# Kernel tuning notes

Hardware: AMD Instinct MI355X
Metric: run time of the kernel (lower is better)

## Reference

```python
import jax, jax.numpy as jnp
import numpy as np

DD = 2.5
GAMMA = 0.005


def setup_inputs() -> dict:
    key = jax.random.key(0)
    k1, k2 = jax.random.split(key)
    B, C, H, W = 8, 32, 512, 512
    K = 16
    features_batch = jax.random.normal(k1, (B, C, H, W), dtype=jnp.float32)
    labels_batch = jax.random.randint(k2, (B, H, W), 0, K, dtype=jnp.int64)
    return {"features_batch": features_batch, "labels_batch": labels_batch, "num_instances": K}


def _per_image_loss(f, lab, K):
    # f: [N, C], lab: [N] int in [0, K)
    counts = jax.ops.segment_sum(jnp.ones(lab.shape, f.dtype), lab, num_segments=K)  # [K]
    sums = jax.ops.segment_sum(f, lab, num_segments=K)                               # [K, C]
    means = sums / counts[:, None]                                                   # [K, C]
    # variance term: mean over pixels of ||x - mean_cluster||^2, summed over clusters
    d2 = jnp.sum((f - means[lab]) ** 2, axis=1)                                      # [N]
    var_loss = jnp.sum(jax.ops.segment_sum(d2, lab, num_segments=K) / counts)
    # pairwise hinge distance term over i<j
    diff2 = jnp.sum((means[:, None, :] - means[None, :, :]) ** 2, axis=-1)           # [K, K]
    eye = jnp.eye(K, dtype=bool)
    dist = jnp.sqrt(jnp.where(eye, 1.0, diff2))  # safe sqrt on diagonal
    hinge = jnp.maximum(2.0 * DD - dist, 0.0) ** 2
    pair_mask = jnp.triu(jnp.ones((K, K), dtype=bool), k=1)
    dist_loss = jnp.sum(jnp.where(pair_mask, hinge, 0.0)) / (K - 1)
    # regularizer: sum of L2 norms of cluster means
    reg_loss = jnp.sum(jnp.sqrt(jnp.sum(means ** 2, axis=-1)))
    return (var_loss + dist_loss + GAMMA * reg_loss) / K


def reference(features_batch, labels_batch, num_instances):
    B, C, H, W = features_batch.shape
    K = int(num_instances)
    feats = jnp.transpose(features_batch, (0, 2, 3, 1)).reshape(B, H * W, C)
    labs = labels_batch.reshape(B, H * W)
    losses = jax.vmap(lambda f, l: _per_image_loss(f, l, K))(feats, labs)  # [B]
    return jnp.sum(losses) / (B + 1)
```

## Files before the change

### kernel.cpp

```cpp
#include <hip/hip_runtime.h>

#define NPIX (512*512)
#define CCH 32
#define KCL 16
#define TPIX 4096
#define BLKT 512
#define STEPS (TPIX/256)
#define WS_STRIDE 544


template<bool WITH_CNT>
__device__ __forceinline__ void run_tile(const float* __restrict__ f0,
    const float* __restrict__ f1, const float* __restrict__ f2,
    const float* __restrict__ f3, const unsigned char* slab, int lane,
    float acc[4][KCL], float* sqa, float* cnt)
{
  #pragma unroll 2
  for (int s = 0; s < STEPS; ++s) {
    const int p = s * 256 + lane * 4;
    const unsigned int labw = *reinterpret_cast<const unsigned int*>(slab + p);
    const float4 a0 = *reinterpret_cast<const float4*>(f0 + p);
    const float4 a1 = *reinterpret_cast<const float4*>(f1 + p);
    const float4 a2 = *reinterpret_cast<const float4*>(f2 + p);
    const float4 a3 = *reinterpret_cast<const float4*>(f3 + p);
    const float va0[4] = {a0.x, a0.y, a0.z, a0.w};
    const float va1[4] = {a1.x, a1.y, a1.z, a1.w};
    const float va2[4] = {a2.x, a2.y, a2.z, a2.w};
    const float va3[4] = {a3.x, a3.y, a3.z, a3.w};
    #pragma unroll
    for (int px = 0; px < 4; ++px) {
      const int lab = (int)((labw >> (8 * px)) & 0xFF);
      const float v0 = va0[px], v1 = va1[px], v2 = va2[px], v3 = va3[px];
      float sq = v0 * v0;
      sq = fmaf(v1, v1, sq);
      sq = fmaf(v2, v2, sq);
      sq = fmaf(v3, v3, sq);
      #pragma unroll
      for (int k = 0; k < KCL; ++k) {
        const float m = (lab == k) ? 1.0f : 0.0f;
        acc[0][k] = fmaf(m, v0, acc[0][k]);
        acc[1][k] = fmaf(m, v1, acc[1][k]);
        acc[2][k] = fmaf(m, v2, acc[2][k]);
        acc[3][k] = fmaf(m, v3, acc[3][k]);
        sqa[k]    = fmaf(m, sq, sqa[k]);
        if (WITH_CNT) cnt[k] += m;
      }
    }
  }
}

#define RS_LEVEL(ARR, HALF, MASK) { \
    const bool hi = (lane & (MASK)) != 0; \
    _Pragma("unroll") \
    for (int j = 0; j < (HALF); ++j) { \
      float send = hi ? ARR[j] : ARR[j + (HALF)]; \
      float recv = __shfl_xor(send, (MASK), 64); \
      ARR[j] = (hi ? ARR[j + (HALF)] : ARR[j]) + recv; \
    } }

__global__ void __launch_bounds__(BLKT)
cl_accum_kernel(const float* __restrict__ feats, const int* __restrict__ labs,
                float* __restrict__ ws)
{
  const int b    = blockIdx.x >> 6;
  const int tile = blockIdx.x & 63;
  const int tid  = threadIdx.x;
  const int wave = tid >> 6;
  const int lane = tid & 63;
  const int px0  = tile * TPIX;

  __shared__ unsigned char slab[TPIX];
  const int* lb = labs + b * NPIX + px0;
  #pragma unroll
  for (int i = 0; i < TPIX / BLKT; ++i)
    slab[tid + i * BLKT] = (unsigned char)lb[tid + i * BLKT];
  __syncthreads();

  const float* fbase = feats + ((long long)b * CCH) * NPIX + px0;
  const float* f0 = fbase + (long long)(wave     ) * NPIX;
  const float* f1 = fbase + (long long)(wave +  8) * NPIX;
  const float* f2 = fbase + (long long)(wave + 16) * NPIX;
  const float* f3 = fbase + (long long)(wave + 24) * NPIX;

  float acc[4][KCL];
  float sqa[KCL], cnt[KCL];
  #pragma unroll
  for (int ch = 0; ch < 4; ++ch)
    #pragma unroll
    for (int k = 0; k < KCL; ++k) acc[ch][k] = 0.f;
  #pragma unroll
  for (int k = 0; k < KCL; ++k) { sqa[k] = 0.f; cnt[k] = 0.f; }

  if (wave == 0) run_tile<true >(f0, f1, f2, f3, slab, lane, acc, sqa, cnt);
  else           run_tile<false>(f0, f1, f2, f3, slab, lane, acc, sqa, cnt);

  float a[64];
  #pragma unroll
  for (int ch = 0; ch < 4; ++ch)
    #pragma unroll
    for (int k = 0; k < KCL; ++k) a[ch * 16 + k] = acc[ch][k];

  RS_LEVEL(a, 32,  1)
  RS_LEVEL(a, 16,  2)
  RS_LEVEL(a,  8,  4)
  RS_LEVEL(a,  4,  8)
  RS_LEVEL(a,  2, 16)
  RS_LEVEL(a,  1, 32)

  {
    const int v6  = (int)(__brev((unsigned)lane) >> 26);
    const int chl = v6 >> 4, k = v6 & 15;
    const int c   = wave + chl * 8;
    atomicAdd(&ws[b * WS_STRIDE + 32 + k * 32 + c], a[0]);
  }

  float bb[32];
  #pragma unroll
  for (int k = 0; k < KCL; ++k) { bb[k] = sqa[k]; bb[16 + k] = cnt[k]; }
  RS_LEVEL(bb, 16,  1)
  RS_LEVEL(bb,  8,  2)
  RS_LEVEL(bb,  4,  4)
  RS_LEVEL(bb,  2,  8)
  RS_LEVEL(bb,  1, 16)
  bb[0] += __shfl_xor(bb[0], 32, 64);
  if (lane < 32) {
    const int v5 = (int)(__brev((unsigned)(lane)) >> 27);
    if (v5 < 16) atomicAdd(&ws[b * WS_STRIDE + 16 + v5], bb[0]);
    else if (wave == 0) atomicAdd(&ws[b * WS_STRIDE + (v5 - 16)], bb[0]);
  }
}

__global__ void __launch_bounds__(512)
cl_finalize_kernel(const float* __restrict__ ws, float* __restrict__ out)
{
  __shared__ float smean[8][KCL][33];
  __shared__ float slossb[8];
  const int tid  = threadIdx.x;
  const int w    = tid >> 6;
  const int lane = tid & 63;
  const float* base = ws + w * WS_STRIDE;

  float m2part = 0.f;
  #pragma unroll
  for (int j = 0; j < 8; ++j) {
    const int idx = lane * 8 + j;
    const int k = idx >> 5, c = idx & 31;
    const float m = base[32 + k * 32 + c] / base[k];
    smean[w][k][c] = m;
    m2part = fmaf(m, m, m2part);
  }
  float varp = -m2part;
  if (lane < 16) varp += base[16 + lane] / base[lane];
  #pragma unroll
  for (int mk = 1; mk < 64; mk <<= 1) varp += __shfl_xor(varp, mk, 64);

  __syncthreads();

  const int kk = lane >> 2, q = lane & 3;
  float n2 = 0.f;
  #pragma unroll
  for (int j = 0; j < 8; ++j) {
    const float m = smean[w][kk][q * 8 + j];
    n2 = fmaf(m, m, n2);
  }
  n2 += __shfl_xor(n2, 1, 64);
  n2 += __shfl_xor(n2, 2, 64);
  float regp = (q == 0) ? sqrtf(n2) : 0.f;
  #pragma unroll
  for (int mk = 1; mk < 64; mk <<= 1) regp += __shfl_xor(regp, mk, 64);

  float hing = 0.f;
  for (int p = lane; p < 120; p += 64) {
    int i = 0, rem = p;
    while (rem >= 15 - i) { rem -= 15 - i; ++i; }
    const int jj = i + 1 + rem;
    float d2 = 0.f;
    #pragma unroll
    for (int c = 0; c < 32; ++c) {
      const float d = smean[w][i][c] - smean[w][jj][c];
      d2 = fmaf(d, d, d2);
    }
    const float h = fmaxf(5.0f - sqrtf(d2), 0.f);
    hing = fmaf(h, h, hing);
  }
  #pragma unroll
  for (int mk = 1; mk < 64; mk <<= 1) hing += __shfl_xor(hing, mk, 64);

  if (lane == 0)
    slossb[w] = (varp + hing * (1.0f / 15.0f) + 0.005f * regp) * (1.0f / 16.0f);
  __syncthreads();
  if (tid == 0) {
    float t = 0.f;
    #pragma unroll
    for (int i = 0; i < 8; ++i) t += slossb[i];
    out[0] = t * (1.0f / 9.0f);
  }
}

extern "C" void kernel_launch(void* const* d_in, const int* in_sizes, int n_in,
                              void* d_out, int out_size, void* d_ws, size_t ws_size,
                              hipStream_t stream)
{
  const float* feats = (const float*)d_in[0];
  const int*   labs  = (const int*)d_in[1];
  float* out = (float*)d_out;
  float* ws  = (float*)d_ws;

  hipMemsetAsync(d_ws, 0, 8 * WS_STRIDE * sizeof(float), stream);
  hipLaunchKernelGGL(cl_accum_kernel, dim3(512), dim3(BLKT), 0, stream,
                     feats, labs, ws);
  hipLaunchKernelGGL(cl_finalize_kernel, dim3(1), dim3(512), 0, stream,
                     ws, out);
}
```

Measured before the change: 77.13 us.

## Distribute label counting across all waves and raise occupancy via launch bounds

Label counts used to be accumulated only by wave 0 inside the main loop, which made that wave do extra work and kept 16 more live registers. Now every thread counts 8 labels from the shared slab after the main loop, and all waves contribute count atomics. __launch_bounds__(BLKT, 4) is added to ask the compiler to limit registers so more blocks can be resident. The risk is register spilling, given the 80+ accumulators per thread, plus more atomics per block.

Result: slower. 130.7 us (+69.4%).

```diff
diff --git a/kernel.cpp b/kernel.cpp
--- a/kernel.cpp
+++ b/kernel.cpp
@@ -9,11 +9,10 @@
 #define WS_STRIDE 544
 
 
-template<bool WITH_CNT>
 __device__ __forceinline__ void run_tile(const float* __restrict__ f0,
     const float* __restrict__ f1, const float* __restrict__ f2,
     const float* __restrict__ f3, const unsigned char* slab, int lane,
-    float acc[4][KCL], float* sqa, float* cnt)
+    float acc[4][KCL], float* sqa)
 {
   #pragma unroll 2
   for (int s = 0; s < STEPS; ++s) {
@@ -43,7 +42,6 @@
         acc[2][k] = fmaf(m, v2, acc[2][k]);
         acc[3][k] = fmaf(m, v3, acc[3][k]);
         sqa[k]    = fmaf(m, sq, sqa[k]);
-        if (WITH_CNT) cnt[k] += m;
       }
     }
   }
@@ -58,7 +56,7 @@
       ARR[j] = (hi ? ARR[j + (HALF)] : ARR[j]) + recv; \
     } }
 
-__global__ void __launch_bounds__(BLKT)
+__global__ void __launch_bounds__(BLKT, 4)
 cl_accum_kernel(const float* __restrict__ feats, const int* __restrict__ labs,
                 float* __restrict__ ws)
 {
@@ -83,16 +81,33 @@
   const float* f3 = fbase + (long long)(wave + 24) * NPIX;
 
   float acc[4][KCL];
-  float sqa[KCL], cnt[KCL];
+  float sqa[KCL];
   #pragma unroll
   for (int ch = 0; ch < 4; ++ch)
     #pragma unroll
     for (int k = 0; k < KCL; ++k) acc[ch][k] = 0.f;
   #pragma unroll
-  for (int k = 0; k < KCL; ++k) { sqa[k] = 0.f; cnt[k] = 0.f; }
-
-  if (wave == 0) run_tile<true >(f0, f1, f2, f3, slab, lane, acc, sqa, cnt);
-  else           run_tile<false>(f0, f1, f2, f3, slab, lane, acc, sqa, cnt);
+  for (int k = 0; k < KCL; ++k) sqa[k] = 0.f;
+
+  run_tile(f0, f1, f2, f3, slab, lane, acc, sqa);
+
+  float cnt[KCL];
+  #pragma unroll
+  for (int k = 0; k < KCL; ++k) cnt[k] = 0.f;
+  {
+    const unsigned int w0 = *reinterpret_cast<const unsigned int*>(slab + tid * 8);
+    const unsigned int w1 = *reinterpret_cast<const unsigned int*>(slab + tid * 8 + 4);
+    #pragma unroll
+    for (int j = 0; j < 4; ++j) {
+      const int l0 = (int)((w0 >> (8 * j)) & 0xFF);
+      const int l1 = (int)((w1 >> (8 * j)) & 0xFF);
+      #pragma unroll
+      for (int k = 0; k < KCL; ++k) {
+        cnt[k] += (l0 == k) ? 1.0f : 0.0f;
+        cnt[k] += (l1 == k) ? 1.0f : 0.0f;
+      }
+    }
+  }
 
   float a[64];
   #pragma unroll
@@ -126,7 +141,7 @@
   if (lane < 32) {
     const int v5 = (int)(__brev((unsigned)(lane)) >> 27);
     if (v5 < 16) atomicAdd(&ws[b * WS_STRIDE + 16 + v5], bb[0]);
-    else if (wave == 0) atomicAdd(&ws[b * WS_STRIDE + (v5 - 16)], bb[0]);
+    else         atomicAdd(&ws[b * WS_STRIDE + (v5 - 16)], bb[0]);
   }
 }
 
```

## Precompute label histogram and fold per-cluster variance into weighted scalar sum

Applied to the files above, without the earlier changes.

Adds a separate histogram kernel that counts labels per image before the main pass. The accumulation kernel then weights each pixel's squared norm by 1/count for its cluster and sums into one scalar, so the 16 per-cluster square-sum and count accumulators and their reductions go away. This lowers register pressure and VALU work in the inner loop, and launch bounds now request 4 waves per SIMD. The cost is an extra kernel launch plus a second read of the labels, and per-pixel weights staged in LDS.

After: 74.42 us. -3.5%, faster.

```diff
diff --git a/kernel.cpp b/kernel.cpp
--- a/kernel.cpp
+++ b/kernel.cpp
@@ -8,17 +8,86 @@
 #define STEPS (TPIX/256)
 #define WS_STRIDE 544
 
-
-template<bool WITH_CNT>
-__device__ __forceinline__ void run_tile(const float* __restrict__ f0,
-    const float* __restrict__ f1, const float* __restrict__ f2,
-    const float* __restrict__ f3, const unsigned char* slab, int lane,
-    float acc[4][KCL], float* sqa, float* cnt)
-{
+#define RS_LEVEL(ARR, HALF, MASK) { \
+    const bool hi = (lane & (MASK)) != 0; \
+    _Pragma("unroll") \
+    for (int j = 0; j < (HALF); ++j) { \
+      float send = hi ? ARR[j] : ARR[j + (HALF)]; \
+      float recv = __shfl_xor(send, (MASK), 64); \
+      ARR[j] = (hi ? ARR[j + (HALF)] : ARR[j]) + recv; \
+    } }
+
+__global__ void __launch_bounds__(512)
+cl_hist_kernel(const int* __restrict__ labs, float* __restrict__ ws)
+{
+  const int b    = blockIdx.x >> 4;
+  const int seg  = blockIdx.x & 15;
+  const int tid  = threadIdx.x;
+  const int lane = tid & 63;
+  const int* base = labs + b * NPIX + seg * (NPIX / 16);
+
+  float c[KCL];
+  #pragma unroll
+  for (int k = 0; k < KCL; ++k) c[k] = 0.f;
+  #pragma unroll 4
+  for (int i = 0; i < 32; ++i) {
+    const int v = base[tid + i * 512];
+    #pragma unroll
+    for (int k = 0; k < KCL; ++k) c[k] += (v == k) ? 1.0f : 0.0f;
+  }
+  RS_LEVEL(c, 8, 1)
+  RS_LEVEL(c, 4, 2)
+  RS_LEVEL(c, 2, 4)
+  RS_LEVEL(c, 1, 8)
+  c[0] += __shfl_xor(c[0], 16, 64);
+  c[0] += __shfl_xor(c[0], 32, 64);
+  if (lane < KCL) {
+    const int v4 = (int)(__brev((unsigned)lane) >> 28);
+    atomicAdd(&ws[b * WS_STRIDE + v4], c[0]);
+  }
+}
+
+__global__ void __launch_bounds__(BLKT, 4)
+cl_accum_kernel(const float* __restrict__ feats, const int* __restrict__ labs,
+                float* __restrict__ ws)
+{
+  const int b    = blockIdx.x >> 6;
+  const int tile = blockIdx.x & 63;
+  const int tid  = threadIdx.x;
+  const int wave = tid >> 6;
+  const int lane = tid & 63;
+  const int px0  = tile * TPIX;
+
+  __shared__ unsigned char slab[TPIX];
+  __shared__ float swei[TPIX];
+  const int* lb = labs + b * NPIX + px0;
+  const float* cntp = ws + b * WS_STRIDE;
+  #pragma unroll
+  for (int i = 0; i < TPIX / BLKT; ++i) {
+    const int v = lb[tid + i * BLKT];
+    slab[tid + i * BLKT] = (unsigned char)v;
+    swei[tid + i * BLKT] = 1.0f / cntp[v];
+  }
+  __syncthreads();
+
+  const float* fbase = feats + ((long long)b * CCH) * NPIX + px0;
+  const float* f0 = fbase + (long long)(wave     ) * NPIX;
+  const float* f1 = fbase + (long long)(wave +  8) * NPIX;
+  const float* f2 = fbase + (long long)(wave + 16) * NPIX;
+  const float* f3 = fbase + (long long)(wave + 24) * NPIX;
+
+  float acc[4][KCL];
+  #pragma unroll
+  for (int ch = 0; ch < 4; ++ch)
+    #pragma unroll
+    for (int k = 0; k < KCL; ++k) acc[ch][k] = 0.f;
+  float wsum = 0.f;
+
   #pragma unroll 2
   for (int s = 0; s < STEPS; ++s) {
     const int p = s * 256 + lane * 4;
     const unsigned int labw = *reinterpret_cast<const unsigned int*>(slab + p);
+    const float4 w4 = *reinterpret_cast<const float4*>(swei + p);
     const float4 a0 = *reinterpret_cast<const float4*>(f0 + p);
     const float4 a1 = *reinterpret_cast<const float4*>(f1 + p);
     const float4 a2 = *reinterpret_cast<const float4*>(f2 + p);
@@ -27,6 +96,7 @@
     const float va1[4] = {a1.x, a1.y, a1.z, a1.w};
     const float va2[4] = {a2.x, a2.y, a2.z, a2.w};
     const float va3[4] = {a3.x, a3.y, a3.z, a3.w};
+    const float vw[4]  = {w4.x, w4.y, w4.z, w4.w};
     #pragma unroll
     for (int px = 0; px < 4; ++px) {
       const int lab = (int)((labw >> (8 * px)) & 0xFF);
@@ -35,6 +105,7 @@
       sq = fmaf(v1, v1, sq);
       sq = fmaf(v2, v2, sq);
       sq = fmaf(v3, v3, sq);
+      wsum = fmaf(vw[px], sq, wsum);
       #pragma unroll
       for (int k = 0; k < KCL; ++k) {
         const float m = (lab == k) ? 1.0f : 0.0f;
@@ -42,57 +113,9 @@
         acc[1][k] = fmaf(m, v1, acc[1][k]);
         acc[2][k] = fmaf(m, v2, acc[2][k]);
         acc[3][k] = fmaf(m, v3, acc[3][k]);
-        sqa[k]    = fmaf(m, sq, sqa[k]);
-        if (WITH_CNT) cnt[k] += m;
       }
     }
   }
-}
-
-#define RS_LEVEL(ARR, HALF, MASK) { \
-    const bool hi = (lane & (MASK)) != 0; \
-    _Pragma("unroll") \
-    for (int j = 0; j < (HALF); ++j) { \
-      float send = hi ? ARR[j] : ARR[j + (HALF)]; \
-      float recv = __shfl_xor(send, (MASK), 64); \
-      ARR[j] = (hi ? ARR[j + (HALF)] : ARR[j]) + recv; \
-    } }
-
-__global__ void __launch_bounds__(BLKT)
-cl_accum_kernel(const float* __restrict__ feats, const int* __restrict__ labs,
-                float* __restrict__ ws)
-{
-  const int b    = blockIdx.x >> 6;
-  const int tile = blockIdx.x & 63;
-  const int tid  = threadIdx.x;
-  const int wave = tid >> 6;
-  const int lane = tid & 63;
-  const int px0  = tile * TPIX;
-
-  __shared__ unsigned char slab[TPIX];
-  const int* lb = labs + b * NPIX + px0;
-  #pragma unroll
-  for (int i = 0; i < TPIX / BLKT; ++i)
-    slab[tid + i * BLKT] = (unsigned char)lb[tid + i * BLKT];
-  __syncthreads();
-
-  const float* fbase = feats + ((long long)b * CCH) * NPIX + px0;
-  const float* f0 = fbase + (long long)(wave     ) * NPIX;
-  const float* f1 = fbase + (long long)(wave +  8) * NPIX;
-  const float* f2 = fbase + (long long)(wave + 16) * NPIX;
-  const float* f3 = fbase + (long long)(wave + 24) * NPIX;
-
-  float acc[4][KCL];
-  float sqa[KCL], cnt[KCL];
-  #pragma unroll
-  for (int ch = 0; ch < 4; ++ch)
-    #pragma unroll
-    for (int k = 0; k < KCL; ++k) acc[ch][k] = 0.f;
-  #pragma unroll
-  for (int k = 0; k < KCL; ++k) { sqa[k] = 0.f; cnt[k] = 0.f; }
-
-  if (wave == 0) run_tile<true >(f0, f1, f2, f3, slab, lane, acc, sqa, cnt);
-  else           run_tile<false>(f0, f1, f2, f3, slab, lane, acc, sqa, cnt);
 
   float a[64];
   #pragma unroll
@@ -114,20 +137,9 @@
     atomicAdd(&ws[b * WS_STRIDE + 32 + k * 32 + c], a[0]);
   }
 
-  float bb[32];
-  #pragma unroll
-  for (int k = 0; k < KCL; ++k) { bb[k] = sqa[k]; bb[16 + k] = cnt[k]; }
-  RS_LEVEL(bb, 16,  1)
-  RS_LEVEL(bb,  8,  2)
-  RS_LEVEL(bb,  4,  4)
-  RS_LEVEL(bb,  2,  8)
-  RS_LEVEL(bb,  1, 16)
-  bb[0] += __shfl_xor(bb[0], 32, 64);
-  if (lane < 32) {
-    const int v5 = (int)(__brev((unsigned)(lane)) >> 27);
-    if (v5 < 16) atomicAdd(&ws[b * WS_STRIDE + 16 + v5], bb[0]);
-    else if (wave == 0) atomicAdd(&ws[b * WS_STRIDE + (v5 - 16)], bb[0]);
-  }
+  #pragma unroll
+  for (int mk = 1; mk < 64; mk <<= 1) wsum += __shfl_xor(wsum, mk, 64);
+  if (lane == 0) atomicAdd(&ws[b * WS_STRIDE + 16], wsum);
 }
 
 __global__ void __launch_bounds__(512)
@@ -150,7 +162,7 @@
     m2part = fmaf(m, m, m2part);
   }
   float varp = -m2part;
-  if (lane < 16) varp += base[16 + lane] / base[lane];
+  if (lane == 0) varp += base[16];
   #pragma unroll
   for (int mk = 1; mk < 64; mk <<= 1) varp += __shfl_xor(varp, mk, 64);
 
@@ -207,6 +219,8 @@
   float* ws  = (float*)d_ws;
 
   hipMemsetAsync(d_ws, 0, 8 * WS_STRIDE * sizeof(float), stream);
+  hipLaunchKernelGGL(cl_hist_kernel, dim3(128), dim3(512), 0, stream,
+                     labs, ws);
   hipLaunchKernelGGL(cl_accum_kernel, dim3(512), dim3(BLKT), 0, stream,
                      feats, labs, ws);
   hipLaunchKernelGGL(cl_finalize_kernel, dim3(1), dim3(512), 0, stream,
```
